# Performance work log

Measured on AMD Instinct MI355X. Metric: run time of the kernel, lower is better.

## Reference

```python
import jax, jax.numpy as jnp
import numpy as np

N_NODES = 50000
N_EDGES = 1600000
IN_DIM = 128
OUT_DIM = 128


def setup_inputs() -> dict:
    key = jax.random.key(0)
    k_h, k_e, k_wm, k_wu, k_bu = jax.random.split(key, 5)
    h = jax.random.normal(k_h, (N_NODES, IN_DIM), dtype=jnp.float32)
    edge_index = jax.random.randint(k_e, (2, N_EDGES), 0, N_NODES, dtype=jnp.int64)
    # nn.Linear weights: W_msg [out, in] no bias; W_upd [out, in+out] with bias
    s1 = 1.0 / np.sqrt(IN_DIM)
    s2 = 1.0 / np.sqrt(IN_DIM + OUT_DIM)
    W_msg = jax.random.uniform(k_wm, (OUT_DIM, IN_DIM), jnp.float32, -s1, s1)
    W_upd = jax.random.uniform(k_wu, (OUT_DIM, IN_DIM + OUT_DIM), jnp.float32, -s2, s2)
    b_upd = jax.random.uniform(k_bu, (OUT_DIM,), jnp.float32, -s2, s2)
    return {"h": h, "edge_index": edge_index, "W_msg": W_msg, "W_upd": W_upd, "b_upd": b_upd}


def reference(h, edge_index, W_msg, W_upd, b_upd):
    src, dst = edge_index[0], edge_index[1]
    # gather -> linear: messages [E, out_dim]
    messages = jnp.einsum("ei,oi->eo", h[src], W_msg)
    # scatter-add aggregation into [N, out_dim]
    agg = jax.ops.segment_sum(messages, dst, num_segments=h.shape[0])
    # concat -> linear -> relu
    hu = jnp.concatenate([h, agg], axis=1)
    return jax.nn.relu(jnp.einsum("ni,oi->no", hu, W_upd) + b_upd)
```

## Files before the change

### kernel.cpp

```cpp
#include <hip/hip_runtime.h>
#include <hip/hip_bf16.h>

#define NN   50000
#define NE   1600000
#define D    128
#define NBK  782
#define CAP2 2816
#define EPB  4096
#define FILLB 391
#define ASTR 136
#define PREP_BLKS 3125
#define WPREP_BLKS 32

typedef __attribute__((ext_vector_type(8))) short short8;
typedef __attribute__((ext_vector_type(4))) float f32x4;

__device__ __forceinline__ unsigned short f2b(float x) {
  unsigned u = __float_as_uint(x);
  u += 0x7fffu + ((u >> 16) & 1u);
  return (unsigned short)(u >> 16);
}
__device__ __forceinline__ float b2f(unsigned v) {
  return __uint_as_float(v << 16);
}
__device__ __forceinline__ float b2fh(unsigned v) {
  return __uint_as_float(v & 0xffff0000u);
}

__global__ __launch_bounds__(512) void fused_k(const float* __restrict__ h,
                                               unsigned short* __restrict__ hb,
                                               int* __restrict__ gcur,
                                               const float* __restrict__ Wm,
                                               const float* __restrict__ Wu,
                                               unsigned short* __restrict__ W1b,
                                               unsigned short* __restrict__ Wcb,
                                               const int* __restrict__ ei,
                                               unsigned* __restrict__ ebuf) {
  __shared__ int cnt[NBK];
  __shared__ int off[NBK];
  __shared__ int nz;
  const int blk = blockIdx.x, tid = threadIdx.x;

  if (blk >= FILLB) {
    if (blk < FILLB + PREP_BLKS) {
      int i = (blk - FILLB) * 512 + tid;
      float4 x = ((const float4*)h)[i];
      ushort4 o;
      o.x = f2b(x.x); o.y = f2b(x.y); o.z = f2b(x.z); o.w = f2b(x.w);
      ((ushort4*)hb)[i] = o;
    } else {
      int t2 = (blk - FILLB - PREP_BLKS) * 512 + tid;
      if (t2 < 16384) {
        int o = t2 >> 7, j = t2 & 127;
        W1b[t2] = f2b(Wu[o * 256 + j]);
        float acc = 0.f;
#pragma unroll 4
        for (int k = 0; k < 128; ++k)
          acc += Wu[o * 256 + 128 + k] * Wm[k * 128 + j];
        Wcb[t2] = f2b(acc);
      }
    }
    return;
  }

  if (tid == 0) nz = 0;
  for (int t = tid; t < NBK; t += 512) cnt[t] = 0;
  __syncthreads();
  if (tid < 256) {
    int idx = 1 + 2 * (tid * (NE / 256));
    if (ei[idx] != 0) atomicOr(&nz, 1);
  }
  __syncthreads();
  const int f = (nz == 0);

  const int e0 = blk * EPB + tid * 8;
  unsigned pk[8]; int bk[8]; int lr[8];
  if (e0 + 8 <= NE) {
    int sv[8], dv[8];
    if (f) {
      const int4* ps = (const int4*)(ei + 2 * (size_t)e0);
      const int4* pd = (const int4*)(ei + 2 * (size_t)NE + 2 * (size_t)e0);
      int4 a = ps[0], b = ps[1], c = ps[2], d = ps[3];
      sv[0]=a.x; sv[1]=a.z; sv[2]=b.x; sv[3]=b.z; sv[4]=c.x; sv[5]=c.z; sv[6]=d.x; sv[7]=d.z;
      a = pd[0]; b = pd[1]; c = pd[2]; d = pd[3];
      dv[0]=a.x; dv[1]=a.z; dv[2]=b.x; dv[3]=b.z; dv[4]=c.x; dv[5]=c.z; dv[6]=d.x; dv[7]=d.z;
    } else {
      const int4* ps = (const int4*)(ei + e0);
      const int4* pd = (const int4*)(ei + (size_t)NE + e0);
      int4 a = ps[0], b = ps[1];
      sv[0]=a.x; sv[1]=a.y; sv[2]=a.z; sv[3]=a.w; sv[4]=b.x; sv[5]=b.y; sv[6]=b.z; sv[7]=b.w;
      a = pd[0]; b = pd[1];
      dv[0]=a.x; dv[1]=a.y; dv[2]=a.z; dv[3]=a.w; dv[4]=b.x; dv[5]=b.y; dv[6]=b.z; dv[7]=b.w;
    }
#pragma unroll
    for (int j = 0; j < 8; ++j) {
      bk[j] = dv[j] >> 6;
      pk[j] = (unsigned)sv[j] | ((unsigned)(dv[j] & 63) << 16);
      lr[j] = atomicAdd(&cnt[bk[j]], 1);
    }
  } else {
    for (int j = 0; j < 8; ++j) {
      int e = e0 + j;
      bk[j] = -1;
      if (e < NE) {
        int src = f ? ei[2 * (size_t)e] : ei[e];
        int dst = f ? ei[2 * ((size_t)NE + e)] : ei[NE + e];
        bk[j] = dst >> 6;
        pk[j] = (unsigned)src | ((unsigned)(dst & 63) << 16);
        lr[j] = atomicAdd(&cnt[bk[j]], 1);
      }
    }
  }
  __syncthreads();
  for (int t = tid; t < NBK; t += 512)
    off[t] = cnt[t] ? atomicAdd(&gcur[t], cnt[t]) : 0;
  __syncthreads();
#pragma unroll
  for (int j = 0; j < 8; ++j) {
    if (bk[j] >= 0) {
      int idx = off[bk[j]] + lr[j];
      if (idx < CAP2) ebuf[(size_t)bk[j] * CAP2 + idx] = pk[j];
    }
  }
}

__global__ __launch_bounds__(512, 4) void sortagg_k(const unsigned* __restrict__ ebuf,
                                                    const int* __restrict__ gcur,
                                                    const unsigned short* __restrict__ hb,
                                                    const unsigned short* __restrict__ W1b,
                                                    const unsigned short* __restrict__ Wcb,
                                                    const float* __restrict__ bias,
                                                    float* __restrict__ out) {
  __shared__ unsigned short srt[CAP2];
  __shared__ __align__(16) unsigned short aggL[64 * ASTR];
  __shared__ int cnt[64];
  __shared__ int ofs[65];
  __shared__ int cur[64];
  const int b = blockIdx.x, tid = threadIdx.x;
  const int lane = tid & 63, wv = tid >> 6;
  if (tid < 64) cnt[tid] = 0;
  __syncthreads();
  const int count = min(gcur[b], CAP2);
  const unsigned* eb = ebuf + (size_t)b * CAP2;
  for (int e = tid; e < count; e += 512)
    atomicAdd(&cnt[eb[e] >> 16], 1);
  __syncthreads();
  if (wv == 0) {
    int v = cnt[lane], s = v;
#pragma unroll
    for (int d = 1; d < 64; d <<= 1) {
      int t = __shfl_up(s, d, 64);
      if (lane >= d) s += t;
    }
    ofs[lane] = s - v;
    cur[lane] = s - v;
    if (lane == 63) ofs[64] = count;
  }
  __syncthreads();
  for (int e = tid; e < count; e += 512) {
    unsigned p = eb[e];
    int slot = atomicAdd(&cur[p >> 16], 1);
    srt[slot] = (unsigned short)(p & 0xffffu);
  }
  __syncthreads();

  const int q = lane >> 4;
  const int r = lane & 15;
  const unsigned short* hbl = hb + r * 8;
#pragma unroll 1
  for (int k = 0; k < 8; ++k) {
    const int n = wv * 8 + k;
    const int beg = ofs[n], end = ofs[n + 1];
    float a0=0.f,a1=0.f,a2=0.f,a3=0.f,a4=0.f,a5=0.f,a6=0.f,a7=0.f;
    int e = beg;
    for (; e + 16 <= end; e += 16) {
      uint4 vv[4];
#pragma unroll
      for (int j = 0; j < 4; ++j)
        vv[j] = *(const uint4*)(hbl + (size_t)srt[e + 4 * j + q] * D);
#pragma unroll
      for (int j = 0; j < 4; ++j) {
        a0 += b2f(vv[j].x & 0xffffu); a1 += b2fh(vv[j].x);
        a2 += b2f(vv[j].y & 0xffffu); a3 += b2fh(vv[j].y);
        a4 += b2f(vv[j].z & 0xffffu); a5 += b2fh(vv[j].z);
        a6 += b2f(vv[j].w & 0xffffu); a7 += b2fh(vv[j].w);
      }
    }
    for (; e < end; e += 4) {
      int edge = e + q;
      int ce = min(edge, end - 1);
      uint4 vv = *(const uint4*)(hbl + (size_t)srt[ce] * D);
      if (edge >= end) { vv.x = 0u; vv.y = 0u; vv.z = 0u; vv.w = 0u; }
      a0 += b2f(vv.x & 0xffffu); a1 += b2fh(vv.x);
      a2 += b2f(vv.y & 0xffffu); a3 += b2fh(vv.y);
      a4 += b2f(vv.z & 0xffffu); a5 += b2fh(vv.z);
      a6 += b2f(vv.w & 0xffffu); a7 += b2fh(vv.w);
    }
    a0 += __shfl_xor(a0, 16, 64); a0 += __shfl_xor(a0, 32, 64);
    a1 += __shfl_xor(a1, 16, 64); a1 += __shfl_xor(a1, 32, 64);
    a2 += __shfl_xor(a2, 16, 64); a2 += __shfl_xor(a2, 32, 64);
    a3 += __shfl_xor(a3, 16, 64); a3 += __shfl_xor(a3, 32, 64);
    a4 += __shfl_xor(a4, 16, 64); a4 += __shfl_xor(a4, 32, 64);
    a5 += __shfl_xor(a5, 16, 64); a5 += __shfl_xor(a5, 32, 64);
    a6 += __shfl_xor(a6, 16, 64); a6 += __shfl_xor(a6, 32, 64);
    a7 += __shfl_xor(a7, 16, 64); a7 += __shfl_xor(a7, 32, 64);
    if (lane < 16) {
      uint4 o;
      o.x = (unsigned)f2b(a0) | ((unsigned)f2b(a1) << 16);
      o.y = (unsigned)f2b(a2) | ((unsigned)f2b(a3) << 16);
      o.z = (unsigned)f2b(a4) | ((unsigned)f2b(a5) << 16);
      o.w = (unsigned)f2b(a6) | ((unsigned)f2b(a7) << 16);
      *(uint4*)(aggL + n * ASTR + r * 8) = o;
    }
  }
  __syncthreads();

  const int rr = lane & 15, g = lane >> 4;
  const int rtile = wv >> 1;
  const int t0 = (wv & 1) * 4;
  const int rowL = rtile * 16 + rr;
  const int nodeA = min(b * 64 + rowL, NN - 1);

  f32x4 acc[4];
#pragma unroll
  for (int t = 0; t < 4; ++t) acc[t] = (f32x4){0.f, 0.f, 0.f, 0.f};

#pragma unroll
  for (int c = 0; c < 8; ++c) {
    const int k0 = (c & 3) * 32 + g * 8;
    short8 a;
    if (c < 4) {
      a = *(const short8*)(hb + (size_t)nodeA * D + k0);
    } else {
      a = *(const short8*)(aggL + rowL * ASTR + k0);
    }
    const unsigned short* W = (c < 4) ? W1b : Wcb;
#pragma unroll
    for (int tt = 0; tt < 4; ++tt) {
      short8 bfr = *(const short8*)(W + (size_t)((t0 + tt) * 16 + rr) * D + k0);
      acc[tt] = __builtin_amdgcn_mfma_f32_16x16x32_bf16(a, bfr, acc[tt], 0, 0, 0);
    }
  }

#pragma unroll
  for (int tt = 0; tt < 4; ++tt) {
    const int col = (t0 + tt) * 16 + rr;
    const float bv = bias[col];
#pragma unroll
    for (int j = 0; j < 4; ++j) {
      const int orow = b * 64 + rtile * 16 + g * 4 + j;
      if (orow < NN) {
        float vv = acc[tt][j] + bv;
        out[(size_t)orow * D + col] = vv > 0.f ? vv : 0.f;
      }
    }
  }
}

extern "C" void kernel_launch(void* const* d_in, const int* in_sizes, int n_in,
                              void* d_out, int out_size, void* d_ws, size_t ws_size,
                              hipStream_t stream) {
  const float* h  = (const float*)d_in[0];
  const int*   ei = (const int*)d_in[1];
  const float* Wm = (const float*)d_in[2];
  const float* Wu = (const float*)d_in[3];
  const float* bu = (const float*)d_in[4];
  float* out = (float*)d_out;

  char* ws = (char*)d_ws;
  unsigned short* hb   = (unsigned short*)(ws);
  unsigned*       ebuf = (unsigned*)(ws + 12800000);
  int*            gcur = (int*)(ws + 21608448);
  unsigned short* W1b  = (unsigned short*)(ws + 21611576 + 8);
  unsigned short* Wcb  = (unsigned short*)(ws + 21644352);

  hipMemsetAsync(gcur, 0, NBK * sizeof(int), stream);
  fused_k<<<FILLB + PREP_BLKS + WPREP_BLKS, 512, 0, stream>>>(
      h, hb, gcur, Wm, Wu, W1b, Wcb, ei, ebuf);
  sortagg_k<<<NBK, 512, 0, stream>>>(ebuf, gcur, hb, W1b, Wcb, bu, out);
}
```

Measured before the change: 121.3 us.

## Sort edges by destination and source chunk, sweep chunks with block barriers for locality

```diff
diff --git a/kernel.cpp b/kernel.cpp
--- a/kernel.cpp
+++ b/kernel.cpp
@@ -133,33 +133,42 @@
                                                     float* __restrict__ out) {
   __shared__ unsigned short srt[CAP2];
   __shared__ __align__(16) unsigned short aggL[64 * ASTR];
-  __shared__ int cnt[64];
-  __shared__ int ofs[65];
-  __shared__ int cur[64];
+  __shared__ int cnt[512];
+  __shared__ int ofs[513];
+  __shared__ int cur[512];
+  __shared__ int wsum[8];
   const int b = blockIdx.x, tid = threadIdx.x;
   const int lane = tid & 63, wv = tid >> 6;
-  if (tid < 64) cnt[tid] = 0;
+  cnt[tid] = 0;
   __syncthreads();
   const int count = min(gcur[b], CAP2);
   const unsigned* eb = ebuf + (size_t)b * CAP2;
-  for (int e = tid; e < count; e += 512)
-    atomicAdd(&cnt[eb[e] >> 16], 1);
-  __syncthreads();
-  if (wv == 0) {
-    int v = cnt[lane], s = v;
+  for (int e = tid; e < count; e += 512) {
+    unsigned p = eb[e];
+    atomicAdd(&cnt[((p >> 16) << 3) | ((p & 0xffffu) >> 13)], 1);
+  }
+  __syncthreads();
+  {
+    int v = cnt[tid], s = v;
 #pragma unroll
     for (int d = 1; d < 64; d <<= 1) {
       int t = __shfl_up(s, d, 64);
       if (lane >= d) s += t;
     }
-    ofs[lane] = s - v;
-    cur[lane] = s - v;
-    if (lane == 63) ofs[64] = count;
+    if (lane == 63) wsum[wv] = s;
+    __syncthreads();
+    int woff = 0;
+    for (int k2 = 0; k2 < wv; ++k2) woff += wsum[k2];
+    int excl = woff + s - v;
+    ofs[tid] = excl;
+    cur[tid] = excl;
+    if (tid == 511) ofs[512] = count;
   }
   __syncthreads();
   for (int e = tid; e < count; e += 512) {
     unsigned p = eb[e];
-    int slot = atomicAdd(&cur[p >> 16], 1);
+    int key = (int)(((p >> 16) << 3) | ((p & 0xffffu) >> 13));
+    int slot = atomicAdd(&cur[key], 1);
     srt[slot] = (unsigned short)(p & 0xffffu);
   }
   __syncthreads();
@@ -167,49 +176,46 @@
   const int q = lane >> 4;
   const int r = lane & 15;
   const unsigned short* hbl = hb + r * 8;
+  float acc[8][8];
+#pragma unroll
+  for (int k = 0; k < 8; ++k)
+#pragma unroll
+    for (int ch = 0; ch < 8; ++ch) acc[k][ch] = 0.f;
+
 #pragma unroll 1
+  for (int c = 0; c < 7; ++c) {
+#pragma unroll
+    for (int k = 0; k < 8; ++k) {
+      const int key = ((wv * 8 + k) << 3) | c;
+      const int beg = ofs[key], end = ofs[key + 1];
+      for (int e = beg; e < end; e += 4) {
+        const int edge = e + q;
+        const int ce = min(edge, end - 1);
+        uint4 vv = *(const uint4*)(hbl + (size_t)srt[ce] * D);
+        if (edge >= end) { vv.x = 0u; vv.y = 0u; vv.z = 0u; vv.w = 0u; }
+        acc[k][0] += b2f(vv.x & 0xffffu); acc[k][1] += b2fh(vv.x);
+        acc[k][2] += b2f(vv.y & 0xffffu); acc[k][3] += b2fh(vv.y);
+        acc[k][4] += b2f(vv.z & 0xffffu); acc[k][5] += b2fh(vv.z);
+        acc[k][6] += b2f(vv.w & 0xffffu); acc[k][7] += b2fh(vv.w);
+      }
+    }
+    __syncthreads();
+  }
+
+#pragma unroll
   for (int k = 0; k < 8; ++k) {
     const int n = wv * 8 + k;
-    const int beg = ofs[n], end = ofs[n + 1];
-    float a0=0.f,a1=0.f,a2=0.f,a3=0.f,a4=0.f,a5=0.f,a6=0.f,a7=0.f;
-    int e = beg;
-    for (; e + 16 <= end; e += 16) {
-      uint4 vv[4];
-#pragma unroll
-      for (int j = 0; j < 4; ++j)
-        vv[j] = *(const uint4*)(hbl + (size_t)srt[e + 4 * j + q] * D);
-#pragma unroll
-      for (int j = 0; j < 4; ++j) {
-        a0 += b2f(vv[j].x & 0xffffu); a1 += b2fh(vv[j].x);
-        a2 += b2f(vv[j].y & 0xffffu); a3 += b2fh(vv[j].y);
-        a4 += b2f(vv[j].z & 0xffffu); a5 += b2fh(vv[j].z);
-        a6 += b2f(vv[j].w & 0xffffu); a7 += b2fh(vv[j].w);
-      }
-    }
-    for (; e < end; e += 4) {
-      int edge = e + q;
-      int ce = min(edge, end - 1);
-      uint4 vv = *(const uint4*)(hbl + (size_t)srt[ce] * D);
-      if (edge >= end) { vv.x = 0u; vv.y = 0u; vv.z = 0u; vv.w = 0u; }
-      a0 += b2f(vv.x & 0xffffu); a1 += b2fh(vv.x);
-      a2 += b2f(vv.y & 0xffffu); a3 += b2fh(vv.y);
-      a4 += b2f(vv.z & 0xffffu); a5 += b2fh(vv.z);
-      a6 += b2f(vv.w & 0xffffu); a7 += b2fh(vv.w);
-    }
-    a0 += __shfl_xor(a0, 16, 64); a0 += __shfl_xor(a0, 32, 64);
-    a1 += __shfl_xor(a1, 16, 64); a1 += __shfl_xor(a1, 32, 64);
-    a2 += __shfl_xor(a2, 16, 64); a2 += __shfl_xor(a2, 32, 64);
-    a3 += __shfl_xor(a3, 16, 64); a3 += __shfl_xor(a3, 32, 64);
-    a4 += __shfl_xor(a4, 16, 64); a4 += __shfl_xor(a4, 32, 64);
-    a5 += __shfl_xor(a5, 16, 64); a5 += __shfl_xor(a5, 32, 64);
-    a6 += __shfl_xor(a6, 16, 64); a6 += __shfl_xor(a6, 32, 64);
-    a7 += __shfl_xor(a7, 16, 64); a7 += __shfl_xor(a7, 32, 64);
+#pragma unroll
+    for (int ch = 0; ch < 8; ++ch) {
+      acc[k][ch] += __shfl_xor(acc[k][ch], 16, 64);
+      acc[k][ch] += __shfl_xor(acc[k][ch], 32, 64);
+    }
     if (lane < 16) {
       uint4 o;
-      o.x = (unsigned)f2b(a0) | ((unsigned)f2b(a1) << 16);
-      o.y = (unsigned)f2b(a2) | ((unsigned)f2b(a3) << 16);
-      o.z = (unsigned)f2b(a4) | ((unsigned)f2b(a5) << 16);
-      o.w = (unsigned)f2b(a6) | ((unsigned)f2b(a7) << 16);
+      o.x = (unsigned)f2b(acc[k][0]) | ((unsigned)f2b(acc[k][1]) << 16);
+      o.y = (unsigned)f2b(acc[k][2]) | ((unsigned)f2b(acc[k][3]) << 16);
+      o.z = (unsigned)f2b(acc[k][4]) | ((unsigned)f2b(acc[k][5]) << 16);
+      o.w = (unsigned)f2b(acc[k][6]) | ((unsigned)f2b(acc[k][7]) << 16);
       *(uint4*)(aggL + n * ASTR + r * 8) = o;
     }
   }
@@ -221,9 +227,9 @@
   const int rowL = rtile * 16 + rr;
   const int nodeA = min(b * 64 + rowL, NN - 1);
 
-  f32x4 acc[4];
-#pragma unroll
-  for (int t = 0; t < 4; ++t) acc[t] = (f32x4){0.f, 0.f, 0.f, 0.f};
+  f32x4 accm[4];
+#pragma unroll
+  for (int t = 0; t < 4; ++t) accm[t] = (f32x4){0.f, 0.f, 0.f, 0.f};
 
 #pragma unroll
   for (int c = 0; c < 8; ++c) {
@@ -238,7 +244,7 @@
 #pragma unroll
     for (int tt = 0; tt < 4; ++tt) {
       short8 bfr = *(const short8*)(W + (size_t)((t0 + tt) * 16 + rr) * D + k0);
-      acc[tt] = __builtin_amdgcn_mfma_f32_16x16x32_bf16(a, bfr, acc[tt], 0, 0, 0);
+      accm[tt] = __builtin_amdgcn_mfma_f32_16x16x32_bf16(a, bfr, accm[tt], 0, 0, 0);
     }
   }
 
@@ -250,7 +256,7 @@
     for (int j = 0; j < 4; ++j) {
       const int orow = b * 64 + rtile * 16 + g * 4 + j;
       if (orow < NN) {
-        float vv = acc[tt][j] + bv;
+        float vv = accm[tt][j] + bv;
         out[(size_t)orow * D + col] = vv > 0.f ? vv : 0.f;
       }
     }
@@ -271,7 +277,7 @@
   unsigned short* hb   = (unsigned short*)(ws);
   unsigned*       ebuf = (unsigned*)(ws + 12800000);
   int*            gcur = (int*)(ws + 21608448);
-  unsigned short* W1b  = (unsigned short*)(ws + 21611576 + 8);
+  unsigned short* W1b  = (unsigned short*)(ws + 21611584);
   unsigned short* Wcb  = (unsigned short*)(ws + 21644352);
 
   hipMemsetAsync(gcur, 0, NBK * sizeof(int), stream);
```

After: 169.4 us. 39.6% more time.
